# Optimization experiments

Measured on AMD Instinct MI355X. Metric: run time of the kernel, lower is better.

## Reference

```python
import jax, jax.numpy as jnp
import numpy as np

B, N, D = 256, 128, 512
NUM_TYPES, NUM_STATS = 6, 8
W_TYPE, W_STATS, W_CORR = 1.0, 1.0, 0.5
LN_EPS = 1e-5


def setup_inputs() -> dict:
    key = jax.random.key(0)
    ks = jax.random.split(key, 20)
    s = 1.0 / np.sqrt(D)
    inp = {
        "column_embeddings": jax.random.normal(ks[0], (B, N, D), jnp.float32),
        "masked_columns": jax.random.bernoulli(ks[1], 0.15, (B, N)),
        "type_targets": jax.random.randint(ks[2], (N,), 0, NUM_TYPES),
        "column_statistics": jax.random.normal(ks[3], (B, N, NUM_STATS), jnp.float32),
        "column_correlations": jnp.tanh(jax.random.normal(ks[4], (B, N, N), jnp.float32)),
        # type head: Linear(D,D) -> GELU -> LayerNorm -> Linear(D,NUM_TYPES)
        "t_W1": jax.random.normal(ks[5], (D, D), jnp.float32) * s,
        "t_b1": jnp.zeros((D,), jnp.float32),
        "t_g": jnp.ones((D,), jnp.float32),
        "t_beta": jnp.zeros((D,), jnp.float32),
        "t_W2": jax.random.normal(ks[6], (D, NUM_TYPES), jnp.float32) * s,
        "t_b2": jnp.zeros((NUM_TYPES,), jnp.float32),
        # stats head
        "s_W1": jax.random.normal(ks[7], (D, D), jnp.float32) * s,
        "s_b1": jnp.zeros((D,), jnp.float32),
        "s_g": jnp.ones((D,), jnp.float32),
        "s_beta": jnp.zeros((D,), jnp.float32),
        "s_W2": jax.random.normal(ks[8], (D, NUM_STATS), jnp.float32) * s,
        "s_b2": jnp.zeros((NUM_STATS,), jnp.float32),
        # bilinear correlation: x_i^T W x_j + b
        "c_W": jax.random.normal(ks[9], (D, D), jnp.float32) * s,
        "c_b": jnp.zeros((), jnp.float32),
    }
    return inp


def _mlp_head(x, W1, b1, g, beta, W2, b2):
    h = jax.nn.gelu(x @ W1 + b1, approximate=False)
    mu = h.mean(-1, keepdims=True)
    var = ((h - mu) ** 2).mean(-1, keepdims=True)
    h = (h - mu) * jax.lax.rsqrt(var + LN_EPS) * g + beta
    return h @ W2 + b2


def _forward(column_embeddings, masked_columns, type_targets,
             column_statistics, column_correlations,
             t_W1, t_b1, t_g, t_beta, t_W2, t_b2,
             s_W1, s_b1, s_g, s_beta, s_W2, s_b2,
             c_W, c_b):
    e = column_embeddings  # [B,N,D]
    type_logits = _mlp_head(e, t_W1, t_b1, t_g, t_beta, t_W2, t_b2)   # [B,N,T]
    stats_preds = _mlp_head(e, s_W1, s_b1, s_g, s_beta, s_W2, s_b2)   # [B,N,S]

    # batched bilinear correlation: tanh(e_i W e_j + b), diag forced to 1
    u = jnp.einsum('bnd,de->bne', e, c_W)            # [B,N,D]
    corr = jnp.tanh(jnp.einsum('bne,bme->bnm', u, e) + c_b)  # [B,N,N]
    eye = jnp.eye(e.shape[1], dtype=corr.dtype)
    corr = corr * (1.0 - eye) + eye

    m = masked_columns.astype(jnp.float32)           # [B,N]
    n_masked = jnp.maximum(m.sum(), 1.0)

    # type loss: masked-mean cross entropy; targets broadcast over batch
    logp = jax.nn.log_softmax(type_logits, axis=-1)
    tgt = jnp.broadcast_to(type_targets[None, :], m.shape)
    ce = -jnp.take_along_axis(logp, tgt[..., None], axis=-1)[..., 0]  # [B,N]
    type_loss = (ce * m).sum() / n_masked

    # stats loss: masked-mean MSE over [B,N,S]
    se = (stats_preds - column_statistics) ** 2
    stats_loss = (se * m[..., None]).sum() / (n_masked * se.shape[-1])

    # correlation loss: mask_expanded = m_i | m_j
    me = jnp.maximum(m[:, :, None], m[:, None, :])   # [B,N,N]
    n_me = jnp.maximum(me.sum(), 1.0)
    ce2 = (corr - column_correlations) ** 2
    correlation_loss = (ce2 * me).sum() / n_me

    total = W_TYPE * type_loss + W_STATS * stats_loss + W_CORR * correlation_loss
    return total


def reference(column_embeddings, masked_columns, type_targets,
              column_statistics, column_correlations,
              t_W1, t_b1, t_g, t_beta, t_W2, t_b2,
              s_W1, s_b1, s_g, s_beta, s_W2, s_b2,
              c_W, c_b):
    return _forward(column_embeddings, masked_columns, type_targets,
                    column_statistics, column_correlations,
                    t_W1, t_b1, t_g, t_beta, t_W2, t_b2,
                    s_W1, s_b1, s_g, s_beta, s_W2, s_b2,
                    c_W, c_b)
```

## Files before the change

kernel.cpp:

```cpp
#include <hip/hip_runtime.h>
#include <math.h>

#define Bx 256
#define Nx 128
#define Dx 512
#define Mx (Bx * Nx)
#define NTYPES 6
#define NSTATS 8
#define LN_EPS 1e-5f
#define CAP 8192

typedef __attribute__((ext_vector_type(8))) short frag8;
typedef __attribute__((ext_vector_type(4))) float f32x4;

__device__ __forceinline__ unsigned short f2bf(float f) {
    unsigned u = __float_as_uint(f);
    u += 0x7fff + ((u >> 16) & 1);
    return (unsigned short)(u >> 16);
}
__device__ __forceinline__ float bf2f(unsigned short s) {
    return __uint_as_float((unsigned)s << 16);
}

#define ASYNC16(g, l) __builtin_amdgcn_global_load_lds(                      \
    (const __attribute__((address_space(1))) void*)(g),                      \
    (__attribute__((address_space(3))) void*)(l), 16, 0, 0)

#define EB_OFF    0ULL
#define U_OFF     33554432ULL
#define HC_OFF    67108864ULL
#define WT_OFF    83886080ULL
#define WTC_OFF   84934656ULL
#define LIST_OFF  85458944ULL
#define CNTS_OFF  85590016ULL
#define PACC_OFF  85591040ULL
#define PCORR_OFF 85593088ULL
#define CNTP_OFF  85594112ULL

__global__ __launch_bounds__(256) void k_prep(
    const float* __restrict__ e, const float* __restrict__ W0,
    const float* __restrict__ W1, const float* __restrict__ W2,
    unsigned short* __restrict__ Eb, unsigned short* __restrict__ Tcmb,
    unsigned short* __restrict__ Tc, const int* __restrict__ m,
    int* __restrict__ list, int* __restrict__ cnts, int* cntp) {
    const int bid = blockIdx.x;
    const int t = threadIdx.x;
    if (bid < 256) {
        const int b = bid;
        const int r = b * Nx + t;
        int v = 0;
        if (t < 128) v = (m[r] != 0) ? 1 : 0;
        const unsigned long long bal = __ballot(v);
        const int wid = t >> 6, lane = t & 63;
        __shared__ int wcnt[2];
        __shared__ int base;
        if (lane == 0 && wid < 2) wcnt[wid] = __popcll(bal);
        __syncthreads();
        const int cnt = wcnt[0] + wcnt[1];
        if (t == 0) {
            base = atomicAdd(cntp, cnt);
            cnts[b] = cnt;
        }
        __syncthreads();
        if (t < 128 && v) {
            const int rank = __popcll(bal & ((1ULL << lane) - 1)) +
                             (wid ? wcnt[0] : 0);
            const int p = base + rank;
            if (p < CAP) list[p] = r;
        }
        return;
    }
    if (bid < 1024) {
        const int lin = (bid - 256) * 256 + t;
        const int mid = lin >> 16;
        const int i4  = (lin & 65535) * 4;
        const int n = i4 >> 9, k = i4 & 511;
        const float* W = (mid == 0) ? W0 : (mid == 1) ? W1 : W2;
        unsigned short* T = (mid == 2) ? Tc : (Tcmb + mid * 262144);
        unsigned short o[4];
#pragma unroll
        for (int j = 0; j < 4; ++j) o[j] = f2bf(W[(k + j) * Dx + n]);
        uint2 u;
        u.x = (unsigned)o[0] | ((unsigned)o[1] << 16);
        u.y = (unsigned)o[2] | ((unsigned)o[3] << 16);
        *(uint2*)(T + i4) = u;
        return;
    }
    const int r = (bid - 1024) * 4 + (t >> 6);
    const int lane = t & 63;
    const float4* src = (const float4*)(e + (size_t)r * Dx);
    const float4 a = src[lane * 2];
    const float4 b = src[lane * 2 + 1];
    unsigned short u[8] = {f2bf(a.x), f2bf(a.y), f2bf(a.z), f2bf(a.w),
                           f2bf(b.x), f2bf(b.y), f2bf(b.z), f2bf(b.w)};
    ((uint4*)(Eb + (size_t)r * Dx))[lane] = *(const uint4*)u;
}

__global__ __launch_bounds__(256) void k_gemms(
    const unsigned short* __restrict__ Eb,
    const unsigned short* __restrict__ Wtc,
    const unsigned short* __restrict__ Wtcmb,
    const float* __restrict__ bias0, const float* __restrict__ bias1,
    unsigned short* __restrict__ U, unsigned short* __restrict__ Hc,
    const int* __restrict__ list, const int* __restrict__ cntp) {
    __shared__ unsigned short As[2 * 4096];
    __shared__ unsigned short Bs[2 * 4096];
    const int bid = blockIdx.x;
    const int t = threadIdx.x;
    const unsigned short* Bt;
    unsigned short* C;
    int row0, col0, ldc, head, ra0, ra1;
    if (bid < 1024) {
        row0 = ((((bid >> 5) << 3) | (bid & 7))) << 7;
        col0 = ((bid >> 3) & 3) << 7;
        Bt = Wtc; C = U; ldc = 512; head = 0;
        ra0 = row0 + (t >> 2);
        ra1 = ra0 + 64;
    } else {
        const int b2 = bid - 1024;
        row0 = (b2 >> 3) << 7;
        const int cnt = min(*cntp, CAP);
        if (row0 >= cnt) return;
        col0 = (b2 & 7) << 7;
        Bt = Wtcmb; C = Hc; ldc = 1024; head = 1;
        ra0 = list[min(row0 + (t >> 2), cnt - 1)];
        ra1 = list[min(row0 + 64 + (t >> 2), cnt - 1)];
    }
    const int w = t >> 6, l = t & 63;
    const int wr = (w >> 1) * 64, wcol = (w & 1) * 64;
    const int quad = l >> 4, mr = l & 15;

    const unsigned short* Ag0 = Eb + (size_t)ra0 * Dx + (t & 3) * 8;
    const unsigned short* Ag1 = Eb + (size_t)ra1 * Dx + (t & 3) * 8;
    const unsigned short* Bg0 = Bt + (size_t)(col0 + (t >> 2)) * Dx + (t & 3) * 8;
    const unsigned short* Bg1 = Bg0 + (size_t)64 * Dx;

    f32x4 acc[4][4] = {};
    for (int k0 = 0; k0 < Dx; k0 += 64) {
        __syncthreads();
#pragma unroll
        for (int s = 0; s < 2; ++s) {
            ASYNC16(Ag0 + k0 + s * 32, As + s * 4096 + t * 8);
            ASYNC16(Ag1 + k0 + s * 32, As + s * 4096 + (t + 256) * 8);
            ASYNC16(Bg0 + k0 + s * 32, Bs + s * 4096 + t * 8);
            ASYNC16(Bg1 + k0 + s * 32, Bs + s * 4096 + (t + 256) * 8);
        }
        __syncthreads();
#pragma unroll
        for (int s = 0; s < 2; ++s) {
            frag8 a[4], b[4];
#pragma unroll
            for (int i = 0; i < 4; ++i)
                a[i] = *(const frag8*)&As[s * 4096 + (wr + i * 16 + mr) * 32 + quad * 8];
#pragma unroll
            for (int j = 0; j < 4; ++j)
                b[j] = *(const frag8*)&Bs[s * 4096 + (wcol + j * 16 + mr) * 32 + quad * 8];
#pragma unroll
            for (int i = 0; i < 4; ++i)
#pragma unroll
                for (int j = 0; j < 4; ++j)
                    acc[i][j] = __builtin_amdgcn_mfma_f32_16x16x32_bf16(
                        a[i], b[j], acc[i][j], 0, 0, 0);
        }
    }
#pragma unroll
    for (int i = 0; i < 4; ++i)
#pragma unroll
        for (int j = 0; j < 4; ++j)
#pragma unroll
            for (int r = 0; r < 4; ++r) {
                const int row = row0 + wr + i * 16 + quad * 4 + r;
                const int col = col0 + wcol + j * 16 + mr;
                float v = acc[i][j][r];
                if (head) {
                    v += (col < 512) ? bias0[col] : bias1[col - 512];
                    v = 0.5f * v * (1.0f + erff(v * 0.70710678118654752f));
                }
                C[(size_t)row * ldc + col] = f2bf(v);
            }
}

__global__ __launch_bounds__(256) void k_tail(
    const unsigned short* __restrict__ U,
    const unsigned short* __restrict__ Eb,
    const float* __restrict__ Ct, const int* __restrict__ m,
    const float* __restrict__ cbp, float* __restrict__ pcorr,
    const unsigned short* __restrict__ Hc,
    const float* __restrict__ tg, const float* __restrict__ tbeta,
    const float* __restrict__ tW2, const float* __restrict__ tb2,
    const float* __restrict__ sg, const float* __restrict__ sbeta,
    const float* __restrict__ sW2, const float* __restrict__ sb2,
    const int* __restrict__ list, const int* __restrict__ cntp,
    const int* __restrict__ tgt, const float* __restrict__ stats,
    float* __restrict__ pacc) {
    __shared__ unsigned short As[2 * 4096];
    __shared__ unsigned short Bs[2 * 4096];
    __shared__ float mloc[128];
    __shared__ float redf[4][2];
    const int t = threadIdx.x;
    const int w = t >> 6, l = t & 63;

    if (blockIdx.x < 256) {
        const int b = blockIdx.x;
        const int wr = (w >> 1) * 64, wcol = (w & 1) * 64;
        const int quad = l >> 4, mr = l & 15;
        if (t < 128) mloc[t] = (m[b * Nx + t] != 0) ? 1.0f : 0.0f;

        const unsigned short* Ub = U + (size_t)b * Nx * Dx;
        const unsigned short* E  = Eb + (size_t)b * Nx * Dx;
        const unsigned short* Ag0 = Ub + (size_t)(t >> 2) * Dx + (t & 3) * 8;
        const unsigned short* Ag1 = Ag0 + (size_t)64 * Dx;
        const unsigned short* Bg0 = E + (size_t)(t >> 2) * Dx + (t & 3) * 8;
        const unsigned short* Bg1 = Bg0 + (size_t)64 * Dx;

        f32x4 acc_r[4][4] = {};
        for (int k0 = 0; k0 < Dx; k0 += 64) {
            __syncthreads();
#pragma unroll
            for (int s = 0; s < 2; ++s) {
                ASYNC16(Ag0 + k0 + s * 32, As + s * 4096 + t * 8);
                ASYNC16(Ag1 + k0 + s * 32, As + s * 4096 + (t + 256) * 8);
                ASYNC16(Bg0 + k0 + s * 32, Bs + s * 4096 + t * 8);
                ASYNC16(Bg1 + k0 + s * 32, Bs + s * 4096 + (t + 256) * 8);
            }
            __syncthreads();
#pragma unroll
            for (int s = 0; s < 2; ++s) {
                frag8 a[4], bfr[4];
#pragma unroll
                for (int i = 0; i < 4; ++i)
                    a[i] = *(const frag8*)&As[s * 4096 + (wr + i * 16 + mr) * 32 + quad * 8];
#pragma unroll
                for (int j = 0; j < 4; ++j)
                    bfr[j] = *(const frag8*)&Bs[s * 4096 + (wcol + j * 16 + mr) * 32 + quad * 8];
#pragma unroll
                for (int i = 0; i < 4; ++i)
#pragma unroll
                    for (int j = 0; j < 4; ++j)
                        acc_r[i][j] = __builtin_amdgcn_mfma_f32_16x16x32_bf16(
                            a[i], bfr[j], acc_r[i][j], 0, 0, 0);
            }
        }
        const float cb = cbp[0];
        float lsum = 0.0f;
#pragma unroll
        for (int i = 0; i < 4; ++i)
#pragma unroll
            for (int j = 0; j < 4; ++j)
#pragma unroll
                for (int r = 0; r < 4; ++r) {
                    const int row = wr + i * 16 + quad * 4 + r;
                    const int col = wcol + j * 16 + mr;
                    float c = (row == col) ? 1.0f : tanhf(acc_r[i][j][r] + cb);
                    const float me = fmaxf(mloc[row], mloc[col]);
                    const float d = c - Ct[((size_t)b * Nx + row) * Nx + col];
                    lsum += me * d * d;
                }
#pragma unroll
        for (int off = 32; off > 0; off >>= 1) lsum += __shfl_down(lsum, off);
        if (l == 0) redf[w][0] = lsum;
        __syncthreads();
        if (t == 0) pcorr[b] = redf[0][0] + redf[1][0] + redf[2][0] + redf[3][0];
        return;
    }

    const int blk = blockIdx.x - 256;
    const int cnt = min(*cntp, CAP);
    float ce_acc = 0.0f, sse_acc = 0.0f;
    for (int idx = blk * 4 + w; idx < cnt; idx += 256 * 4) {
        const int r = list[idx];
        const uint4 ut = ((const uint4*)(Hc + (size_t)idx * 1024))[l];
        const uint4 us = ((const uint4*)(Hc + (size_t)idx * 1024 + 512))[l];
        float a[8], b8[8];
        {
            const unsigned uu[4] = {ut.x, ut.y, ut.z, ut.w};
            const unsigned vv[4] = {us.x, us.y, us.z, us.w};
#pragma unroll
            for (int j = 0; j < 4; ++j) {
                a[2 * j]      = bf2f((unsigned short)(uu[j] & 0xffff));
                a[2 * j + 1]  = bf2f((unsigned short)(uu[j] >> 16));
                b8[2 * j]     = bf2f((unsigned short)(vv[j] & 0xffff));
                b8[2 * j + 1] = bf2f((unsigned short)(vv[j] >> 16));
            }
        }
        float st = 0, qt = 0, ss = 0, qs = 0;
#pragma unroll
        for (int j = 0; j < 8; ++j) {
            st += a[j]; qt += a[j] * a[j];
            ss += b8[j]; qs += b8[j] * b8[j];
        }
#pragma unroll
        for (int off = 32; off > 0; off >>= 1) {
            st += __shfl_xor(st, off); qt += __shfl_xor(qt, off);
            ss += __shfl_xor(ss, off); qs += __shfl_xor(qs, off);
        }
        const float mt = st * (1.0f / Dx);
        const float rt = rsqrtf(qt * (1.0f / Dx) - mt * mt + LN_EPS);
        const float ms = ss * (1.0f / Dx);
        const float rs = rsqrtf(qs * (1.0f / Dx) - ms * ms + LN_EPS);

        const int c0 = l * 8;
        float tp[6] = {}, sp[8] = {};
#pragma unroll
        for (int j = 0; j < 8; ++j) {
            const int c = c0 + j;
            const float nt = (a[j] - mt) * rt * tg[c] + tbeta[c];
#pragma unroll
            for (int k = 0; k < 6; ++k) tp[k] += nt * tW2[c * 6 + k];
            const float ns = (b8[j] - ms) * rs * sg[c] + sbeta[c];
#pragma unroll
            for (int k = 0; k < 8; ++k) sp[k] += ns * sW2[c * 8 + k];
        }
#pragma unroll
        for (int k = 0; k < 6; ++k)
#pragma unroll
            for (int off = 32; off > 0; off >>= 1) tp[k] += __shfl_down(tp[k], off);
#pragma unroll
        for (int k = 0; k < 8; ++k)
#pragma unroll
            for (int off = 32; off > 0; off >>= 1) sp[k] += __shfl_down(sp[k], off);

        if (l == 0) {
            float lg[6];
#pragma unroll
            for (int k = 0; k < 6; ++k) lg[k] = tp[k] + tb2[k];
            float mx = lg[0];
#pragma unroll
            for (int k = 1; k < 6; ++k) mx = fmaxf(mx, lg[k]);
            float se = 0.0f;
#pragma unroll
            for (int k = 0; k < 6; ++k) se += expf(lg[k] - mx);
            ce_acc += -(lg[tgt[r & (Nx - 1)]] - mx - logf(se));
            float sse = 0.0f;
#pragma unroll
            for (int k = 0; k < 8; ++k) {
                const float d = sp[k] + sb2[k] - stats[(size_t)r * NSTATS + k];
                sse += d * d;
            }
            sse_acc += sse;
        }
    }
    if (l == 0) { redf[w][0] = ce_acc; redf[w][1] = sse_acc; }
    __syncthreads();
    if (t == 0) {
        pacc[2 * blk]     = redf[0][0] + redf[1][0] + redf[2][0] + redf[3][0];
        pacc[2 * blk + 1] = redf[0][1] + redf[1][1] + redf[2][1] + redf[3][1];
    }
}

__global__ __launch_bounds__(256) void k_final(
    const float* __restrict__ pacc, const float* __restrict__ pcorr,
    const int* __restrict__ cnts, const int* __restrict__ cntp,
    float* __restrict__ out) {
    const int t = threadIdx.x, w = t >> 6, lane = t & 63;
    float ce = pacc[2 * t], sse = pacc[2 * t + 1], co = pcorr[t];
    const int c = cnts[t];
    float me = (float)(Nx * Nx) - (float)((Nx - c) * (Nx - c));
#pragma unroll
    for (int off = 32; off > 0; off >>= 1) {
        ce += __shfl_down(ce, off);
        sse += __shfl_down(sse, off);
        co += __shfl_down(co, off);
        me += __shfl_down(me, off);
    }
    __shared__ float red[4][4];
    if (lane == 0) {
        red[w][0] = ce; red[w][1] = sse; red[w][2] = co; red[w][3] = me;
    }
    __syncthreads();
    if (t == 0) {
        const float CE = red[0][0] + red[1][0] + red[2][0] + red[3][0];
        const float SSE = red[0][1] + red[1][1] + red[2][1] + red[3][1];
        const float CO = red[0][2] + red[1][2] + red[2][2] + red[3][2];
        const float ME = red[0][3] + red[1][3] + red[2][3] + red[3][3];
        const float nm = fmaxf((float)*cntp, 1.0f);
        const float nme = fmaxf(ME, 1.0f);
        out[0] = CE / nm + SSE / (nm * (float)NSTATS) + 0.5f * CO / nme;
    }
}

extern "C" void kernel_launch(void* const* d_in, const int* in_sizes, int n_in,
                              void* d_out, int out_size, void* d_ws, size_t ws_size,
                              hipStream_t stream) {
    const float* e      = (const float*)d_in[0];
    const int*   mcols  = (const int*)d_in[1];
    const int*   ttgt   = (const int*)d_in[2];
    const float* stats  = (const float*)d_in[3];
    const float* corrT  = (const float*)d_in[4];
    const float* tW1    = (const float*)d_in[5];
    const float* tb1    = (const float*)d_in[6];
    const float* tg     = (const float*)d_in[7];
    const float* tbeta  = (const float*)d_in[8];
    const float* tW2    = (const float*)d_in[9];
    const float* tb2    = (const float*)d_in[10];
    const float* sW1    = (const float*)d_in[11];
    const float* sb1    = (const float*)d_in[12];
    const float* sg     = (const float*)d_in[13];
    const float* sbeta  = (const float*)d_in[14];
    const float* sW2    = (const float*)d_in[15];
    const float* sb2    = (const float*)d_in[16];
    const float* cW     = (const float*)d_in[17];
    const float* cb     = (const float*)d_in[18];
    float* out = (float*)d_out;

    char* ws = (char*)d_ws;
    unsigned short* Eb    = (unsigned short*)(ws + EB_OFF);
    unsigned short* U     = (unsigned short*)(ws + U_OFF);
    unsigned short* Hc    = (unsigned short*)(ws + HC_OFF);
    unsigned short* Wtcmb = (unsigned short*)(ws + WT_OFF);
    unsigned short* Wtc   = (unsigned short*)(ws + WTC_OFF);
    int*   list  = (int*)(ws + LIST_OFF);
    int*   cnts  = (int*)(ws + CNTS_OFF);
    float* pacc  = (float*)(ws + PACC_OFF);
    float* pcorr = (float*)(ws + PCORR_OFF);
    int*   cntp  = (int*)(ws + CNTP_OFF);

    hipMemsetAsync(cntp, 0, sizeof(int), stream);
    k_prep<<<9216, 256, 0, stream>>>(e, tW1, sW1, cW, Eb, Wtcmb, Wtc, mcols,
                                     list, cnts, cntp);
    k_gemms<<<1536, 256, 0, stream>>>(Eb, Wtc, Wtcmb, tb1, sb1, U, Hc, list, cntp);
    k_tail<<<512, 256, 0, stream>>>(U, Eb, corrT, mcols, cb, pcorr,
                                    Hc, tg, tbeta, tW2, tb2, sg, sbeta, sW2, sb2,
                                    list, cntp, ttgt, stats, pacc);
    k_final<<<1, 256, 0, stream>>>(pacc, pcorr, cnts, cntp, out);
}
```

Measured before the change: 239.5 us.

## Double-buffer LDS tiles with XOR-swizzled layout in both GEMM kernels

Both MFMA GEMM loops now use two 64-wide K buffers in LDS. The next K tile is issued asynchronously while the current one is consumed, so only one barrier is needed per iteration instead of two. Each row in LDS is laid out contiguously over 64 K elements with an XOR swizzle of the 16-byte chunk index, which is meant to avoid bank conflicts on the fragment reads. This doubles the LDS footprint to 64 KB per block, which may lower occupancy.

```diff
diff --git a/kernel.cpp b/kernel.cpp
--- a/kernel.cpp
+++ b/kernel.cpp
@@ -25,6 +25,12 @@
 #define ASYNC16(g, l) __builtin_amdgcn_global_load_lds(                      \
     (const __attribute__((address_space(1))) void*)(g),                      \
     (__attribute__((address_space(3))) void*)(l), 16, 0, 0)
+
+#define STAGE8(buf, k0)                                                      \
+  { _Pragma("unroll") for (int s_ = 0; s_ < 4; ++s_) {                       \
+      ASYNC16(pA[s_] + (k0), As + (buf) * 8192 + s_ * 2048 + t * 8);         \
+      ASYNC16(pB[s_] + (k0), Bs + (buf) * 8192 + s_ * 2048 + t * 8);         \
+  } }
 
 #define EB_OFF    0ULL
 #define U_OFF     33554432ULL
@@ -103,58 +109,60 @@
     const float* __restrict__ bias0, const float* __restrict__ bias1,
     unsigned short* __restrict__ U, unsigned short* __restrict__ Hc,
     const int* __restrict__ list, const int* __restrict__ cntp) {
-    __shared__ unsigned short As[2 * 4096];
-    __shared__ unsigned short Bs[2 * 4096];
+    __shared__ unsigned short As[2 * 8192];
+    __shared__ unsigned short Bs[2 * 8192];
     const int bid = blockIdx.x;
     const int t = threadIdx.x;
-    const unsigned short* Bt;
+    const unsigned short* Bbase;
     unsigned short* C;
-    int row0, col0, ldc, head, ra0, ra1;
+    int row0, col0, ldc, head;
+    int raA[4];
     if (bid < 1024) {
         row0 = ((((bid >> 5) << 3) | (bid & 7))) << 7;
         col0 = ((bid >> 3) & 3) << 7;
-        Bt = Wtc; C = U; ldc = 512; head = 0;
-        ra0 = row0 + (t >> 2);
-        ra1 = ra0 + 64;
+        Bbase = Wtc; C = U; ldc = 512; head = 0;
+#pragma unroll
+        for (int s = 0; s < 4; ++s) raA[s] = row0 + s * 32 + (t >> 3);
     } else {
         const int b2 = bid - 1024;
         row0 = (b2 >> 3) << 7;
         const int cnt = min(*cntp, CAP);
         if (row0 >= cnt) return;
         col0 = (b2 & 7) << 7;
-        Bt = Wtcmb; C = Hc; ldc = 1024; head = 1;
-        ra0 = list[min(row0 + (t >> 2), cnt - 1)];
-        ra1 = list[min(row0 + 64 + (t >> 2), cnt - 1)];
+        Bbase = Wtcmb; C = Hc; ldc = 1024; head = 1;
+#pragma unroll
+        for (int s = 0; s < 4; ++s)
+            raA[s] = list[min(row0 + s * 32 + (t >> 3), cnt - 1)];
+    }
+    const int kq = (t & 7) ^ ((t >> 3) & 7);
+    const unsigned short* pA[4];
+    const unsigned short* pB[4];
+#pragma unroll
+    for (int s = 0; s < 4; ++s) {
+        pA[s] = Eb + (size_t)raA[s] * Dx + kq * 8;
+        pB[s] = Bbase + (size_t)(col0 + s * 32 + (t >> 3)) * Dx + kq * 8;
     }
     const int w = t >> 6, l = t & 63;
     const int wr = (w >> 1) * 64, wcol = (w & 1) * 64;
     const int quad = l >> 4, mr = l & 15;
-
-    const unsigned short* Ag0 = Eb + (size_t)ra0 * Dx + (t & 3) * 8;
-    const unsigned short* Ag1 = Eb + (size_t)ra1 * Dx + (t & 3) * 8;
-    const unsigned short* Bg0 = Bt + (size_t)(col0 + (t >> 2)) * Dx + (t & 3) * 8;
-    const unsigned short* Bg1 = Bg0 + (size_t)64 * Dx;
+    const int rx = mr & 7;
 
     f32x4 acc[4][4] = {};
-    for (int k0 = 0; k0 < Dx; k0 += 64) {
-        __syncthreads();
-#pragma unroll
-        for (int s = 0; s < 2; ++s) {
-            ASYNC16(Ag0 + k0 + s * 32, As + s * 4096 + t * 8);
-            ASYNC16(Ag1 + k0 + s * 32, As + s * 4096 + (t + 256) * 8);
-            ASYNC16(Bg0 + k0 + s * 32, Bs + s * 4096 + t * 8);
-            ASYNC16(Bg1 + k0 + s * 32, Bs + s * 4096 + (t + 256) * 8);
-        }
-        __syncthreads();
-#pragma unroll
-        for (int s = 0; s < 2; ++s) {
+    STAGE8(0, 0);
+    __syncthreads();
+    for (int kt = 0; kt < 8; ++kt) {
+        const int cur = kt & 1;
+        if (kt < 7) STAGE8(cur ^ 1, (kt + 1) * 64);
+#pragma unroll
+        for (int ss = 0; ss < 2; ++ss) {
+            const int co = ((ss * 4 + quad) ^ rx) * 8;
             frag8 a[4], b[4];
 #pragma unroll
             for (int i = 0; i < 4; ++i)
-                a[i] = *(const frag8*)&As[s * 4096 + (wr + i * 16 + mr) * 32 + quad * 8];
+                a[i] = *(const frag8*)&As[cur * 8192 + (wr + i * 16 + mr) * 64 + co];
 #pragma unroll
             for (int j = 0; j < 4; ++j)
-                b[j] = *(const frag8*)&Bs[s * 4096 + (wcol + j * 16 + mr) * 32 + quad * 8];
+                b[j] = *(const frag8*)&Bs[cur * 8192 + (wcol + j * 16 + mr) * 64 + co];
 #pragma unroll
             for (int i = 0; i < 4; ++i)
 #pragma unroll
@@ -162,6 +170,7 @@
                     acc[i][j] = __builtin_amdgcn_mfma_f32_16x16x32_bf16(
                         a[i], b[j], acc[i][j], 0, 0, 0);
         }
+        if (kt < 7) __syncthreads();
     }
 #pragma unroll
     for (int i = 0; i < 4; ++i)
@@ -193,8 +202,8 @@
     const int* __restrict__ list, const int* __restrict__ cntp,
     const int* __restrict__ tgt, const float* __restrict__ stats,
     float* __restrict__ pacc) {
-    __shared__ unsigned short As[2 * 4096];
-    __shared__ unsigned short Bs[2 * 4096];
+    __shared__ unsigned short As[2 * 8192];
+    __shared__ unsigned short Bs[2 * 8192];
     __shared__ float mloc[128];
     __shared__ float redf[4][2];
     const int t = threadIdx.x;
@@ -204,35 +213,35 @@
         const int b = blockIdx.x;
         const int wr = (w >> 1) * 64, wcol = (w & 1) * 64;
         const int quad = l >> 4, mr = l & 15;
+        const int rx = mr & 7;
         if (t < 128) mloc[t] = (m[b * Nx + t] != 0) ? 1.0f : 0.0f;
 
-        const unsigned short* Ub = U + (size_t)b * Nx * Dx;
-        const unsigned short* E  = Eb + (size_t)b * Nx * Dx;
-        const unsigned short* Ag0 = Ub + (size_t)(t >> 2) * Dx + (t & 3) * 8;
-        const unsigned short* Ag1 = Ag0 + (size_t)64 * Dx;
-        const unsigned short* Bg0 = E + (size_t)(t >> 2) * Dx + (t & 3) * 8;
-        const unsigned short* Bg1 = Bg0 + (size_t)64 * Dx;
+        const int kq = (t & 7) ^ ((t >> 3) & 7);
+        const unsigned short* pA[4];
+        const unsigned short* pB[4];
+#pragma unroll
+        for (int s = 0; s < 4; ++s) {
+            const size_t rr = (size_t)b * Nx + s * 32 + (t >> 3);
+            pA[s] = U + rr * Dx + kq * 8;
+            pB[s] = Eb + rr * Dx + kq * 8;
+        }
 
         f32x4 acc_r[4][4] = {};
-        for (int k0 = 0; k0 < Dx; k0 += 64) {
-            __syncthreads();
-#pragma unroll
-            for (int s = 0; s < 2; ++s) {
-                ASYNC16(Ag0 + k0 + s * 32, As + s * 4096 + t * 8);
-                ASYNC16(Ag1 + k0 + s * 32, As + s * 4096 + (t + 256) * 8);
-                ASYNC16(Bg0 + k0 + s * 32, Bs + s * 4096 + t * 8);
-                ASYNC16(Bg1 + k0 + s * 32, Bs + s * 4096 + (t + 256) * 8);
-            }
-            __syncthreads();
-#pragma unroll
-            for (int s = 0; s < 2; ++s) {
+        STAGE8(0, 0);
+        __syncthreads();
+        for (int kt = 0; kt < 8; ++kt) {
+            const int cur = kt & 1;
+            if (kt < 7) STAGE8(cur ^ 1, (kt + 1) * 64);
+#pragma unroll
+            for (int ss = 0; ss < 2; ++ss) {
+                const int co = ((ss * 4 + quad) ^ rx) * 8;
                 frag8 a[4], bfr[4];
 #pragma unroll
                 for (int i = 0; i < 4; ++i)
-                    a[i] = *(const frag8*)&As[s * 4096 + (wr + i * 16 + mr) * 32 + quad * 8];
+                    a[i] = *(const frag8*)&As[cur * 8192 + (wr + i * 16 + mr) * 64 + co];
 #pragma unroll
                 for (int j = 0; j < 4; ++j)
-                    bfr[j] = *(const frag8*)&Bs[s * 4096 + (wcol + j * 16 + mr) * 32 + quad * 8];
+                    bfr[j] = *(const frag8*)&Bs[cur * 8192 + (wcol + j * 16 + mr) * 64 + co];
 #pragma unroll
                 for (int i = 0; i < 4; ++i)
 #pragma unroll
@@ -240,6 +249,7 @@
                         acc_r[i][j] = __builtin_amdgcn_mfma_f32_16x16x32_bf16(
                             a[i], bfr[j], acc_r[i][j], 0, 0, 0);
             }
+            if (kt < 7) __syncthreads();
         }
         const float cb = cbp[0];
         float lsum = 0.0f;
```

Measured after the change: 238.7 us. Within noise of the previous version (-0.3%).

## Pipeline GEMM K-loop with 4-stage async LDS buffers and XOR swizzle

Applied to the files above, without the earlier changes.

Replaces the load-then-compute K loop, which had two block barriers per step, in both the projection GEMM kernel and the bilinear correlation GEMM. Each now runs a 4-deep ring of LDS stages, issuing async global-to-LDS loads three stages ahead and waiting with a counted vmcnt plus one barrier per step. It also XOR-swizzles the k-chunk position within each LDS row to cut bank conflicts on fragment reads, and raises wave priority around the MFMA bursts. Shared memory per block doubles, which may lower occupancy.

```diff
diff --git a/kernel.cpp b/kernel.cpp
--- a/kernel.cpp
+++ b/kernel.cpp
@@ -25,6 +25,36 @@
 #define ASYNC16(g, l) __builtin_amdgcn_global_load_lds(                      \
     (const __attribute__((address_space(1))) void*)(g),                      \
     (__attribute__((address_space(3))) void*)(l), 16, 0, 0)
+
+
+#define GSTAGE(b, ph)                                                        \
+  {                                                                          \
+    ASYNC16(pA0 + (ph) * 32, As + (b) * 4096 + t * 8);                       \
+    ASYNC16(pA1 + (ph) * 32, As + (b) * 4096 + 2048 + t * 8);                \
+    ASYNC16(pB0 + (ph) * 32, Bs + (b) * 4096 + t * 8);                       \
+    ASYNC16(pB1 + (ph) * 32, Bs + (b) * 4096 + 2048 + t * 8);                \
+  }
+
+#define GCOMPUTE(pb)                                                         \
+  {                                                                          \
+    const int lb = (pb) * 4096;                                              \
+    frag8 af[4], bfv[4];                                                     \
+    _Pragma("unroll") for (int i = 0; i < 4; ++i)                            \
+        af[i] = *(const frag8*)&As[lb + (wr + i * 16 + mr) * 32 + co];       \
+    _Pragma("unroll") for (int j = 0; j < 4; ++j)                            \
+        bfv[j] = *(const frag8*)&Bs[lb + (wcol + j * 16 + mr) * 32 + co];    \
+    __builtin_amdgcn_s_setprio(1);                                           \
+    _Pragma("unroll") for (int i = 0; i < 4; ++i)                            \
+      _Pragma("unroll") for (int j = 0; j < 4; ++j)                          \
+        acc[i][j] = __builtin_amdgcn_mfma_f32_16x16x32_bf16(                 \
+            af[i], bfv[j], acc[i][j], 0, 0, 0);                              \
+    __builtin_amdgcn_s_setprio(0);                                           \
+  }
+
+#define GBAR(NIMM)                                                           \
+    asm volatile("s_waitcnt vmcnt(" #NIMM ")" ::: "memory");                 \
+    __builtin_amdgcn_s_barrier();                                            \
+    __builtin_amdgcn_sched_barrier(0);
 
 #define EB_OFF    0ULL
 #define U_OFF     33554432ULL
@@ -103,66 +133,51 @@
     const float* __restrict__ bias0, const float* __restrict__ bias1,
     unsigned short* __restrict__ U, unsigned short* __restrict__ Hc,
     const int* __restrict__ list, const int* __restrict__ cntp) {
-    __shared__ unsigned short As[2 * 4096];
-    __shared__ unsigned short Bs[2 * 4096];
+    __shared__ unsigned short As[4 * 4096];
+    __shared__ unsigned short Bs[4 * 4096];
     const int bid = blockIdx.x;
     const int t = threadIdx.x;
-    const unsigned short* Bt;
+    const unsigned short* Bbase;
     unsigned short* C;
     int row0, col0, ldc, head, ra0, ra1;
     if (bid < 1024) {
         row0 = ((((bid >> 5) << 3) | (bid & 7))) << 7;
         col0 = ((bid >> 3) & 3) << 7;
-        Bt = Wtc; C = U; ldc = 512; head = 0;
+        Bbase = Wtc; C = U; ldc = 512; head = 0;
         ra0 = row0 + (t >> 2);
-        ra1 = ra0 + 64;
+        ra1 = row0 + 64 + (t >> 2);
     } else {
         const int b2 = bid - 1024;
         row0 = (b2 >> 3) << 7;
         const int cnt = min(*cntp, CAP);
         if (row0 >= cnt) return;
         col0 = (b2 & 7) << 7;
-        Bt = Wtcmb; C = Hc; ldc = 1024; head = 1;
+        Bbase = Wtcmb; C = Hc; ldc = 1024; head = 1;
         ra0 = list[min(row0 + (t >> 2), cnt - 1)];
         ra1 = list[min(row0 + 64 + (t >> 2), cnt - 1)];
     }
+    const int kq = (t & 3) ^ ((t >> 3) & 3);
+    const unsigned short* pA0 = Eb + (size_t)ra0 * Dx + kq * 8;
+    const unsigned short* pA1 = Eb + (size_t)ra1 * Dx + kq * 8;
+    const unsigned short* pB0 = Bbase + (size_t)(col0 + (t >> 2)) * Dx + kq * 8;
+    const unsigned short* pB1 = Bbase + (size_t)(col0 + 64 + (t >> 2)) * Dx + kq * 8;
+
     const int w = t >> 6, l = t & 63;
     const int wr = (w >> 1) * 64, wcol = (w & 1) * 64;
     const int quad = l >> 4, mr = l & 15;
-
-    const unsigned short* Ag0 = Eb + (size_t)ra0 * Dx + (t & 3) * 8;
-    const unsigned short* Ag1 = Eb + (size_t)ra1 * Dx + (t & 3) * 8;
-    const unsigned short* Bg0 = Bt + (size_t)(col0 + (t >> 2)) * Dx + (t & 3) * 8;
-    const unsigned short* Bg1 = Bg0 + (size_t)64 * Dx;
+    const int co = (quad ^ ((mr >> 1) & 3)) * 8;
 
     f32x4 acc[4][4] = {};
-    for (int k0 = 0; k0 < Dx; k0 += 64) {
-        __syncthreads();
-#pragma unroll
-        for (int s = 0; s < 2; ++s) {
-            ASYNC16(Ag0 + k0 + s * 32, As + s * 4096 + t * 8);
-            ASYNC16(Ag1 + k0 + s * 32, As + s * 4096 + (t + 256) * 8);
-            ASYNC16(Bg0 + k0 + s * 32, Bs + s * 4096 + t * 8);
-            ASYNC16(Bg1 + k0 + s * 32, Bs + s * 4096 + (t + 256) * 8);
-        }
-        __syncthreads();
-#pragma unroll
-        for (int s = 0; s < 2; ++s) {
-            frag8 a[4], b[4];
-#pragma unroll
-            for (int i = 0; i < 4; ++i)
-                a[i] = *(const frag8*)&As[s * 4096 + (wr + i * 16 + mr) * 32 + quad * 8];
-#pragma unroll
-            for (int j = 0; j < 4; ++j)
-                b[j] = *(const frag8*)&Bs[s * 4096 + (wcol + j * 16 + mr) * 32 + quad * 8];
-#pragma unroll
-            for (int i = 0; i < 4; ++i)
-#pragma unroll
-                for (int j = 0; j < 4; ++j)
-                    acc[i][j] = __builtin_amdgcn_mfma_f32_16x16x32_bf16(
-                        a[i], b[j], acc[i][j], 0, 0, 0);
-        }
-    }
+    GSTAGE(0, 0); GSTAGE(1, 1); GSTAGE(2, 2);
+    for (int p = 0; p < 13; ++p) {
+        GBAR(8);
+        GSTAGE((p + 3) & 3, p + 3);
+        GCOMPUTE(p & 3);
+    }
+    GBAR(8); GCOMPUTE(1);
+    GBAR(4); GCOMPUTE(2);
+    GBAR(0); GCOMPUTE(3);
+
 #pragma unroll
     for (int i = 0; i < 4; ++i)
 #pragma unroll
@@ -193,8 +208,8 @@
     const int* __restrict__ list, const int* __restrict__ cntp,
     const int* __restrict__ tgt, const float* __restrict__ stats,
     float* __restrict__ pacc) {
-    __shared__ unsigned short As[2 * 4096];
-    __shared__ unsigned short Bs[2 * 4096];
+    __shared__ unsigned short As[4 * 4096];
+    __shared__ unsigned short Bs[4 * 4096];
     __shared__ float mloc[128];
     __shared__ float redf[4][2];
     const int t = threadIdx.x;
@@ -204,43 +219,28 @@
         const int b = blockIdx.x;
         const int wr = (w >> 1) * 64, wcol = (w & 1) * 64;
         const int quad = l >> 4, mr = l & 15;
+        const int co = (quad ^ ((mr >> 1) & 3)) * 8;
         if (t < 128) mloc[t] = (m[b * Nx + t] != 0) ? 1.0f : 0.0f;
-
-        const unsigned short* Ub = U + (size_t)b * Nx * Dx;
-        const unsigned short* E  = Eb + (size_t)b * Nx * Dx;
-        const unsigned short* Ag0 = Ub + (size_t)(t >> 2) * Dx + (t & 3) * 8;
-        const unsigned short* Ag1 = Ag0 + (size_t)64 * Dx;
-        const unsigned short* Bg0 = E + (size_t)(t >> 2) * Dx + (t & 3) * 8;
-        const unsigned short* Bg1 = Bg0 + (size_t)64 * Dx;
-
-        f32x4 acc_r[4][4] = {};
-        for (int k0 = 0; k0 < Dx; k0 += 64) {
-            __syncthreads();
-#pragma unroll
-            for (int s = 0; s < 2; ++s) {
-                ASYNC16(Ag0 + k0 + s * 32, As + s * 4096 + t * 8);
-                ASYNC16(Ag1 + k0 + s * 32, As + s * 4096 + (t + 256) * 8);
-                ASYNC16(Bg0 + k0 + s * 32, Bs + s * 4096 + t * 8);
-                ASYNC16(Bg1 + k0 + s * 32, Bs + s * 4096 + (t + 256) * 8);
-            }
-            __syncthreads();
-#pragma unroll
-            for (int s = 0; s < 2; ++s) {
-                frag8 a[4], bfr[4];
-#pragma unroll
-                for (int i = 0; i < 4; ++i)
-                    a[i] = *(const frag8*)&As[s * 4096 + (wr + i * 16 + mr) * 32 + quad * 8];
-#pragma unroll
-                for (int j = 0; j < 4; ++j)
-                    bfr[j] = *(const frag8*)&Bs[s * 4096 + (wcol + j * 16 + mr) * 32 + quad * 8];
-#pragma unroll
-                for (int i = 0; i < 4; ++i)
-#pragma unroll
-                    for (int j = 0; j < 4; ++j)
-                        acc_r[i][j] = __builtin_amdgcn_mfma_f32_16x16x32_bf16(
-                            a[i], bfr[j], acc_r[i][j], 0, 0, 0);
-            }
-        }
+        asm volatile("s_waitcnt lgkmcnt(0)" ::: "memory");
+
+        const int kq = (t & 3) ^ ((t >> 3) & 3);
+        const size_t rb = (size_t)b * Nx;
+        const unsigned short* pA0 = U + (rb + (t >> 2)) * Dx + kq * 8;
+        const unsigned short* pA1 = U + (rb + 64 + (t >> 2)) * Dx + kq * 8;
+        const unsigned short* pB0 = Eb + (rb + (t >> 2)) * Dx + kq * 8;
+        const unsigned short* pB1 = Eb + (rb + 64 + (t >> 2)) * Dx + kq * 8;
+
+        f32x4 acc[4][4] = {};
+        GSTAGE(0, 0); GSTAGE(1, 1); GSTAGE(2, 2);
+        for (int p = 0; p < 13; ++p) {
+            GBAR(8);
+            GSTAGE((p + 3) & 3, p + 3);
+            GCOMPUTE(p & 3);
+        }
+        GBAR(8); GCOMPUTE(1);
+        GBAR(4); GCOMPUTE(2);
+        GBAR(0); GCOMPUTE(3);
+
         const float cb = cbp[0];
         float lsum = 0.0f;
 #pragma unroll
@@ -251,7 +251,7 @@
                 for (int r = 0; r < 4; ++r) {
                     const int row = wr + i * 16 + quad * 4 + r;
                     const int col = wcol + j * 16 + mr;
-                    float c = (row == col) ? 1.0f : tanhf(acc_r[i][j][r] + cb);
+                    float c = (row == col) ? 1.0f : tanhf(acc[i][j][r] + cb);
                     const float me = fmaxf(mloc[row], mloc[col]);
                     const float d = c - Ct[((size_t)b * Nx + row) * Nx + col];
                     lsum += me * d * d;
```

After: 239.9 us. No clear change (+0.2%).
